# Kernel optimization log

Measured on AMD Instinct MI355X. Metric: run time of the kernel, lower is better.

The kernel has to match this reference:

```python
import jax, jax.numpy as jnp
import numpy as np

N = 20000
E = 320000
C = 16   # in_channels
G = 8    # growth_channels
H = 16   # kernel MLP hidden = RDB in_channels
DIM = 3
OMEGA = 100.0
BETA = 0.2


def _u(k, shape, s):
    return jax.random.uniform(k, shape, jnp.float32, -s, s)


def setup_inputs() -> dict:
    key = jax.random.key(0)
    ks = jax.random.split(key, 64)
    x = jax.random.normal(ks[0], (N, C), jnp.float32)
    pos = jax.random.normal(ks[1], (N, DIM), jnp.float32)
    # random edges with no self loops (add_remaining_self_loops appends them in reference)
    src = jax.random.randint(ks[2], (E,), 0, N)
    off = jax.random.randint(ks[3], (E,), 1, N)
    dst = (src + off) % N
    edge_index = jnp.stack([src, dst])
    d = {"x": x, "edge_index": edge_index, "pos": pos}
    ins = [C, C + G, C + 2 * G]
    outs = [G, G, C]
    i = 4
    for ci, (cin, cout) in enumerate(zip(ins, outs), 1):
        # SineLayer weights: uniform(-1/in_features, 1/in_features); biases ~ torch Linear default
        d[f"c{ci}_w0"] = _u(ks[i], (H, DIM + 1), 1.0 / (DIM + 1)); i += 1
        d[f"c{ci}_b0"] = _u(ks[i], (H,), 1.0 / np.sqrt(DIM + 1)); i += 1
        d[f"c{ci}_w1"] = _u(ks[i], (H, H), 1.0 / H); i += 1
        d[f"c{ci}_b1"] = _u(ks[i], (H,), 1.0 / np.sqrt(H)); i += 1
        d[f"c{ci}_w2"] = _u(ks[i], (H, H), 1.0 / H); i += 1
        d[f"c{ci}_b2"] = _u(ks[i], (H,), 1.0 / np.sqrt(H)); i += 1
        # final Linear(hidden -> in_size), stored transposed as [in_size, hidden]
        d[f"c{ci}_wl"] = _u(ks[i], (cin, H), 1.0 / np.sqrt(H)); i += 1
        d[f"c{ci}_bl"] = _u(ks[i], (cin,), 1.0 / np.sqrt(H)); i += 1
        d[f"c{ci}_bias"] = jnp.zeros((1, cout), jnp.float32); i += 1
    return d


def _edge_feat(pos, src, dst):
    # rel_pos = pos[dst] - pos[src]; spherical (rho, theta/pi, phi/pi), NaN at rho=0 -> 0
    rel = pos[dst] - pos[src]                              # [E,3]
    sq = jnp.sum(rel * rel, axis=1)
    zero = sq <= 0.0                                       # self loops
    rho = jnp.where(zero, 0.0, jnp.sqrt(jnp.where(zero, 1.0, sq)))
    theta = jnp.arctan2(jnp.where(zero, 0.0, rel[:, 1]), jnp.where(zero, 1.0, rel[:, 0]))
    phi = jnp.arcsin(jnp.clip(jnp.where(zero, 0.0, rel[:, 2]) / jnp.where(zero, 1.0, rho), -1.0, 1.0))
    return jnp.stack([rho, theta / jnp.pi, phi / jnp.pi], axis=1)  # [E,3]


def _gconv(feat, x, src, dst, n, out_ch, w0, b0, w1, b1, w2, b2, wl, bl, bias):
    # vectorized over output channels: channel index c is the 4th input of sin0
    base = feat @ w0[:, :3].T + b0                          # [E,H]
    ch = jnp.arange(out_ch, dtype=feat.dtype)               # [O]
    h = jnp.sin(OMEGA * (base[:, None, :] + ch[None, :, None] * w0[:, 3]))   # [E,O,H]
    h = jnp.sin(OMEGA * (jnp.einsum('eoh,gh->eog', h, w1) + b1))
    h = jnp.sin(OMEGA * (jnp.einsum('eoh,gh->eog', h, w2) + b2))
    xj = x[src]                                             # [E,in]
    # msg[e,o] = (Wl h[e,o] + bl) . x_j[e]  ==  h[e,o] . (Wl^T x_j[e]) + bl . x_j[e]
    msg = jnp.einsum('eoh,eh->eo', h, xj @ wl) + (xj @ bl)[:, None]
    return jax.ops.segment_sum(msg, dst, num_segments=n) + bias


def reference(x, edge_index, pos,
              c1_w0, c1_b0, c1_w1, c1_b1, c1_w2, c1_b2, c1_wl, c1_bl, c1_bias,
              c2_w0, c2_b0, c2_w1, c2_b1, c2_w2, c2_b2, c2_wl, c2_bl, c2_bias,
              c3_w0, c3_b0, c3_w1, c3_b1, c3_w2, c3_b2, c3_wl, c3_bl, c3_bias):
    n = x.shape[0]
    loop = jnp.arange(n, dtype=edge_index.dtype)
    src = jnp.concatenate([edge_index[0], loop])
    dst = jnp.concatenate([edge_index[1], loop])
    feat = _edge_feat(pos, src, dst)
    x1 = jax.nn.selu(_gconv(feat, x, src, dst, n, G, c1_w0, c1_b0, c1_w1, c1_b1, c1_w2, c1_b2, c1_wl, c1_bl, c1_bias))
    x2 = jax.nn.selu(_gconv(feat, jnp.concatenate([x, x1], 1), src, dst, n, G, c2_w0, c2_b0, c2_w1, c2_b1, c2_w2, c2_b2, c2_wl, c2_bl, c2_bias))
    x3 = jax.nn.selu(_gconv(feat, jnp.concatenate([x, x1, x2], 1), src, dst, n, C, c3_w0, c3_b0, c3_w1, c3_b1, c3_w2, c3_b2, c3_wl, c3_bl, c3_bias))
    return x + BETA * x3
```

## Files before the change

kernel.cpp:

```cpp
#include <hip/hip_runtime.h>
#include <math.h>

#define N_NODES 20000
#define N_EDGES 320000
#define HID 16
#define OMEGA 100.0f
#define BETA 0.2f
#define REVC 0.15915494309189535f

#define OFF_W0I 0
#define OFF_B1  64
#define OFF_B2  80
#define OFF_A2  128
#define OFF_WLH 384
#define OFF_WLL 640
#define OFF_AO  896
#define OFF_H2V 9088
#define P_SIZE  9472

typedef float  f32x4 __attribute__((ext_vector_type(4)));
typedef short  s16x8 __attribute__((ext_vector_type(8)));

__device__ __forceinline__ float sinrev(float x) { return __builtin_amdgcn_sinf(x); }
__device__ __forceinline__ float cosrev(float x) { return __builtin_amdgcn_cosf(x); }
__device__ __forceinline__ float fract_f(float x) { return __builtin_amdgcn_fractf(x); }

__device__ __forceinline__ float selu_f(float v) {
    const float a  = 1.6732632423543772f;
    const float sc = 1.0507009873554805f;
    return sc * (v > 0.f ? v : a * expm1f(v));
}

__device__ __forceinline__ f32x4 mfma16(s16x8 a, s16x8 b, f32x4 c) {
    return __builtin_amdgcn_mfma_f32_16x16x32_bf16(a, b, c, 0, 0, 0);
}

__device__ __forceinline__ unsigned pk_hi(float a, float b) {
    return (__float_as_uint(b) & 0xFFFF0000u) | (__float_as_uint(a) >> 16);
}
__device__ __forceinline__ float lo_of(float a) {
    return a - __uint_as_float(__float_as_uint(a) & 0xFFFF0000u);
}

union U4 { uint4 v; s16x8 s; };

struct PrepArgs {
    const float* w0[3]; const float* b0[3]; const float* w1[3]; const float* b1[3];
    const float* w2[3]; const float* b2[3]; const float* wl[3];
    float* P[3];
};

__global__ __launch_bounds__(256) void prep_kernel(PrepArgs A)
{
    const int INS[3]  = {16, 24, 32};
    const int OUTS[3] = {8, 8, 16};
    int c = blockIdx.x;
    int IN = INS[c], OUT = OUTS[c];
    const float* w0 = A.w0[c]; const float* b0 = A.b0[c];
    const float* w1 = A.w1[c]; const float* b1 = A.b1[c];
    const float* w2 = A.w2[c]; const float* b2 = A.b2[c];
    const float* wl = A.wl[c];
    float* P = A.P[c];
    unsigned* Pu = (unsigned*)P;

    __shared__ float W1s[256], W2s[256], cosB[256], sinB[256], w0c[16];
    int t = threadIdx.x;
    const float s = OMEGA * REVC;
    W1s[t] = s * w1[t];
    W2s[t] = s * w2[t];
    if (t < 16) w0c[t] = s * w0[t * 4 + 3];
    __syncthreads();

    if (t < 64) { int h = t >> 2, k = t & 3; P[t] = (k < 3) ? s * w0[h * 4 + k] : s * b0[h]; }
    if (t >= 64 && t < 80)  P[t] = s * b1[t - 64];
    if (t >= 80 && t < 96)  P[t] = s * b2[t - 80];

    if (t < OUT * 16) {
        int o = t >> 4, h = t & 15;
        float ang = fract_f((float)o * w0c[h]);
        cosB[t] = cosrev(ang);
        sinB[t] = sinrev(ang);
    }
    __syncthreads();

    if (t < 64) {
        int g = t & 15, q = t >> 4;
        float w[4], l[4];
#pragma unroll
        for (int j = 0; j < 4; j++) { w[j] = W2s[g * 16 + 4 * q + j]; l[j] = lo_of(w[j]); }
        ((uint4*)(Pu + OFF_A2))[t] = make_uint4(pk_hi(w[0], w[1]), pk_hi(w[2], w[3]),
                                                pk_hi(l[0], l[1]), pk_hi(l[2], l[3]));
    }
    if (t >= 64 && t < 128) {
        int lane = t - 64, g = lane & 15, q = lane >> 4;
        float v[8], l[8];
#pragma unroll
        for (int e = 0; e < 8; e++) {
            int i = 8 * q + e;
            v[e] = (i < IN) ? wl[i * 16 + g] : 0.f;
            l[e] = lo_of(v[e]);
        }
        ((uint4*)(Pu + OFF_WLH))[lane] = make_uint4(pk_hi(v[0], v[1]), pk_hi(v[2], v[3]),
                                                    pk_hi(v[4], v[5]), pk_hi(v[6], v[7]));
        ((uint4*)(Pu + OFF_WLL))[lane] = make_uint4(pk_hi(l[0], l[1]), pk_hi(l[2], l[3]),
                                                    pk_hi(l[4], l[5]), pk_hi(l[6], l[7]));
    }
    for (int idx = t; idx < OUT * 64; idx += 256) {
        int o = idx >> 6, lane = idx & 63, g = lane & 15, q = lane >> 4;
        float v[8], l[8];
#pragma unroll
        for (int e = 0; e < 8; e++) {
            int k = 8 * q + e;
            float a = (k < 16) ? W1s[g * 16 + k] * cosB[o * 16 + k]
                               : W1s[g * 16 + (k - 16)] * sinB[o * 16 + (k - 16)];
            v[e] = a; l[e] = lo_of(a);
        }
        ((uint4*)(Pu + OFF_AO + o * 512))[lane] =
            make_uint4(pk_hi(v[0], v[1]), pk_hi(v[2], v[3]), pk_hi(v[4], v[5]), pk_hi(v[6], v[7]));
        ((uint4*)(Pu + OFF_AO + o * 512 + 256))[lane] =
            make_uint4(pk_hi(l[0], l[1]), pk_hi(l[2], l[3]), pk_hi(l[4], l[5]), pk_hi(l[6], l[7]));
    }
    if (t < OUT) {
        float oc = (float)t;
        float h0[HID], h1[HID];
#pragma unroll
        for (int h = 0; h < HID; h++)
            h0[h] = sinrev(fract_f(fmaf(oc, w0c[h], s * b0[h])));
#pragma unroll
        for (int g = 0; g < HID; g++) {
            float sa = s * b1[g];
#pragma unroll
            for (int h = 0; h < HID; h++) sa += h0[h] * W1s[g * HID + h];
            h1[g] = sinrev(sa);
        }
#pragma unroll
        for (int g = 0; g < HID; g++) {
            float sa = s * b2[g];
#pragma unroll
            for (int h = 0; h < HID; h++) sa += h1[h] * W2s[g * HID + h];
            P[OFF_H2V + t * HID + g] = sinrev(sa);
        }
    }
}

__global__ __launch_bounds__(256) void fused_pre_kernel(
    const int* __restrict__ ei, const float* __restrict__ pos,
    const float* __restrict__ x,
    float4* __restrict__ feat, float* __restrict__ xcat,
    const float* __restrict__ wl1, const float* __restrict__ bl1,
    float* __restrict__ tb, float* __restrict__ blxb)
{
    int b = blockIdx.x;
    if (b < 1250) {
        int e = b * 256 + threadIdx.x;
        if (e >= N_EDGES) return;
        int s = ei[e], d = ei[N_EDGES + e];
        float rx = pos[d * 3 + 0] - pos[s * 3 + 0];
        float ry = pos[d * 3 + 1] - pos[s * 3 + 1];
        float rz = pos[d * 3 + 2] - pos[s * 3 + 2];
        float sq = rx * rx + ry * ry + rz * rz;
        float4 f = make_float4(0.f, 0.f, 0.f, 0.f);
        if (sq > 0.f) {
            float rho = sqrtf(sq);
            float th  = atan2f(ry, rx);
            float ph  = asinf(fminf(fmaxf(rz / rho, -1.f), 1.f));
            const float inv_pi = 0.31830988618379067f;
            f = make_float4(rho, th * inv_pi, ph * inv_pi, 0.f);
        }
        feat[e] = f;
    } else if (b < 2500) {
        int i = (b - 1250) * 256 + threadIdx.x;
        if (i >= N_NODES * 16) return;
        int n = i >> 4, cc = i & 15;
        xcat[n * 32 + cc] = x[i];
    } else {
        int n = (b - 2500) * 256 + threadIdx.x;
        if (n >= N_NODES) return;
        float tn[HID];
#pragma unroll
        for (int h = 0; h < HID; h++) tn[h] = 0.f;
        float bx = 0.f;
#pragma unroll
        for (int i = 0; i < 16; i++) {
            float xi = x[n * 16 + i];
            bx += bl1[i] * xi;
#pragma unroll
            for (int h = 0; h < HID; h++) tn[h] += wl1[i * 16 + h] * xi;
        }
#pragma unroll
        for (int h = 0; h < HID; h++) tb[n * 16 + h] = tn[h];
        blxb[n] = bx;
    }
}

template<int OUT, int IN>
__global__ __launch_bounds__(256) void conv_kernel(
    const int* __restrict__ ei, const float4* __restrict__ feat,
    const float* __restrict__ xcat, const float* __restrict__ P,
    const float* __restrict__ bl, float* __restrict__ acc)
{
    constexpr int L2O = (OUT == 16) ? 4 : 3;
    constexpr int EPI = 64 / OUT;
    constexpr int NI  = 16 / EPI;

    __shared__ float sm[4][16 * 17];
    const unsigned* Pu = (const unsigned*)P;
    int wslot = threadIdx.x >> 6;
    int wid  = (blockIdx.x * 256 + threadIdx.x) >> 6;
    int lane = threadIdx.x & 63;
    int e16 = lane & 15, q = lane >> 4;
    int e = wid * 16 + e16;
    int src = ei[e];
    int dst = ei[N_EDGES + e];
    float4 f = feat[e];

    float tr[8];
    {
        const float4* w0i = (const float4*)P;
        int hb = (q & 1) * 8;
#pragma unroll
        for (int j = 0; j < 8; j++) {
            float4 w = w0i[hb + j];
            float ang = fract_f(w.w + f.x * w.x + f.y * w.y + f.z * w.z);
            tr[j] = (q < 2) ? sinrev(ang) : cosrev(ang);
        }
    }
    U4 Bh, Bl;
    Bh.v = make_uint4(pk_hi(tr[0], tr[1]), pk_hi(tr[2], tr[3]),
                      pk_hi(tr[4], tr[5]), pk_hi(tr[6], tr[7]));
    Bl.v = make_uint4(pk_hi(lo_of(tr[0]), lo_of(tr[1])), pk_hi(lo_of(tr[2]), lo_of(tr[3])),
                      pk_hi(lo_of(tr[4]), lo_of(tr[5])), pk_hi(lo_of(tr[6]), lo_of(tr[7])));

    float xv[8];
#pragma unroll
    for (int j = 0; j < 8; j++) xv[j] = 0.f;
    if (8 * q < IN) {
        const f32x4* xr = (const f32x4*)(xcat + src * 32 + 8 * q);
        f32x4 x0 = xr[0], x1 = xr[1];
        xv[0] = x0[0]; xv[1] = x0[1]; xv[2] = x0[2]; xv[3] = x0[3];
        xv[4] = x1[0]; xv[5] = x1[1]; xv[6] = x1[2]; xv[7] = x1[3];
    }
    U4 Xh, Xl;
    Xh.v = make_uint4(pk_hi(xv[0], xv[1]), pk_hi(xv[2], xv[3]),
                      pk_hi(xv[4], xv[5]), pk_hi(xv[6], xv[7]));
    Xl.v = make_uint4(pk_hi(lo_of(xv[0]), lo_of(xv[1])), pk_hi(lo_of(xv[2]), lo_of(xv[3])),
                      pk_hi(lo_of(xv[4]), lo_of(xv[5])), pk_hi(lo_of(xv[6]), lo_of(xv[7])));
    U4 WLh, WLl;
    WLh.v = ((const uint4*)(Pu + OFF_WLH))[lane];
    WLl.v = ((const uint4*)(Pu + OFF_WLL))[lane];
    f32x4 T = {0.f, 0.f, 0.f, 0.f};
    T = mfma16(WLh.s, Xh.s, T);
    T = mfma16(WLh.s, Xl.s, T);
    T = mfma16(WLl.s, Xh.s, T);

    float bx = 0.f;
    if (8 * q < IN) {
        const f32x4* blr = (const f32x4*)(bl + 8 * q);
        f32x4 b0v = blr[0], b1v = blr[1];
        bx = b0v[0] * xv[0] + b0v[1] * xv[1] + b0v[2] * xv[2] + b0v[3] * xv[3]
           + b1v[0] * xv[4] + b1v[1] * xv[5] + b1v[2] * xv[6] + b1v[3] * xv[7];
    }
    bx += __shfl_xor(bx, 16);
    bx += __shfl_xor(bx, 32);

    U4 A2; A2.v = ((const uint4*)(Pu + OFF_A2))[lane];
    f32x4 c1 = *(const f32x4*)(P + OFF_B1 + 4 * q);
    f32x4 c2 = *(const f32x4*)(P + OFF_B2 + 4 * q);

#pragma unroll 2
    for (int o = 0; o < OUT; ++o) {
        U4 Ah, Al;
        Ah.v = ((const uint4*)(Pu + OFF_AO + o * 512))[lane];
        Al.v = ((const uint4*)(Pu + OFF_AO + o * 512 + 256))[lane];
        f32x4 D = c1;
        D = mfma16(Ah.s, Bh.s, D);
        D = mfma16(Ah.s, Bl.s, D);
        D = mfma16(Al.s, Bh.s, D);
        float h1[4];
#pragma unroll
        for (int j = 0; j < 4; j++) h1[j] = sinrev(D[j]);
        unsigned p0 = pk_hi(h1[0], h1[1]), p1 = pk_hi(h1[2], h1[3]);
        unsigned l0 = pk_hi(lo_of(h1[0]), lo_of(h1[1])), l1 = pk_hi(lo_of(h1[2]), lo_of(h1[3]));
        U4 Ph, Pl;
        Ph.v = make_uint4(p0, p1, p0, p1);
        Pl.v = make_uint4(l0, l1, l0, l1);
        f32x4 D2 = c2;
        D2 = mfma16(A2.s, Ph.s, D2);
        D2 = mfma16(A2.s, Pl.s, D2);
        float m = sinrev(D2[0]) * T[0] + sinrev(D2[1]) * T[1]
                + sinrev(D2[2]) * T[2] + sinrev(D2[3]) * T[3];
        m += __shfl_xor(m, 16);
        m += __shfl_xor(m, 32);
        if (lane < 16) sm[wslot][o * 17 + e16] = m + bx;
    }

    int oo = lane & (OUT - 1);
    int el = lane >> L2O;
#pragma unroll
    for (int j = 0; j < NI; j++) {
        int ej = j * EPI + el;
        int dj = __shfl(dst, ej);
        atomicAdd(&acc[dj * OUT + oo], sm[wslot][oo * 17 + ej]);
    }
}

template<int OUT, int CO>
__global__ __launch_bounds__(256) void finish_mid_kernel(
    const float* __restrict__ acc, const float* __restrict__ bias,
    const float* __restrict__ h2v,
    float* __restrict__ tb, float* __restrict__ blxb,
    float* __restrict__ xcat,
    const float* __restrict__ wlN, const float* __restrict__ blN)
{
    int n = blockIdx.x * 256 + threadIdx.x;
    if (n >= N_NODES) return;
    float trr[HID];
#pragma unroll
    for (int h = 0; h < HID; h++) trr[h] = tb[n * 16 + h];
    float bx = blxb[n];
    float xrow[CO + OUT];
#pragma unroll
    for (int i = 0; i < CO; i++) xrow[i] = xcat[n * 32 + i];
#pragma unroll
    for (int o = 0; o < OUT; o++) {
        float m = bx;
#pragma unroll
        for (int h = 0; h < HID; h++) m += h2v[o * 16 + h] * trr[h];
        float v = selu_f(acc[n * OUT + o] + bias[o] + m);
        xrow[CO + o] = v;
        xcat[n * 32 + CO + o] = v;
    }
    float tn[HID];
#pragma unroll
    for (int h = 0; h < HID; h++) tn[h] = 0.f;
    float bxn = 0.f;
#pragma unroll
    for (int i = 0; i < CO + OUT; i++) {
        float xi = xrow[i];
        bxn += blN[i] * xi;
#pragma unroll
        for (int h = 0; h < HID; h++) tn[h] += wlN[i * 16 + h] * xi;
    }
#pragma unroll
    for (int h = 0; h < HID; h++) tb[n * 16 + h] = tn[h];
    blxb[n] = bxn;
}

__global__ __launch_bounds__(256) void finish_out_kernel(
    const float* __restrict__ acc, const float* __restrict__ bias,
    const float* __restrict__ h2v,
    const float* __restrict__ tb, const float* __restrict__ blxb,
    const float* __restrict__ x, float* __restrict__ out)
{
    int n = blockIdx.x * 256 + threadIdx.x;
    if (n >= N_NODES) return;
    float trr[HID];
#pragma unroll
    for (int h = 0; h < HID; h++) trr[h] = tb[n * 16 + h];
    float bx = blxb[n];
#pragma unroll
    for (int c = 0; c < 16; c++) {
        float m = bx;
#pragma unroll
        for (int h = 0; h < HID; h++) m += h2v[c * 16 + h] * trr[h];
        out[n * 16 + c] = x[n * 16 + c] + BETA * selu_f(acc[n * 16 + c] + bias[c] + m);
    }
}

extern "C" void kernel_launch(void* const* d_in, const int* in_sizes, int n_in,
                              void* d_out, int out_size, void* d_ws, size_t ws_size,
                              hipStream_t stream)
{
    const float* x   = (const float*)d_in[0];
    const int*   ei  = (const int*)d_in[1];
    const float* pos = (const float*)d_in[2];

    const float* W[27];
    for (int i = 0; i < 27; i++) W[i] = (const float*)d_in[3 + i];

    float* ws    = (float*)d_ws;
    float4* feat = (float4*)ws;
    float* xcat  = ws + (size_t)N_EDGES * 4;
    float* acc1  = xcat + (size_t)N_NODES * 32;
    float* acc2  = acc1 + (size_t)N_NODES * 8;
    float* acc3  = acc2 + (size_t)N_NODES * 8;
    float* P1    = acc3 + (size_t)N_NODES * 16;
    float* P2    = P1 + P_SIZE;
    float* P3    = P2 + P_SIZE;
    float* tb    = P3 + P_SIZE;
    float* blxb  = tb + (size_t)N_NODES * 16;
    float* out   = (float*)d_out;

    hipMemsetAsync(acc1, 0, (size_t)N_NODES * 32 * sizeof(float), stream);

    PrepArgs pa;
    for (int c = 0; c < 3; c++) {
        pa.w0[c] = W[9 * c + 0]; pa.b0[c] = W[9 * c + 1];
        pa.w1[c] = W[9 * c + 2]; pa.b1[c] = W[9 * c + 3];
        pa.w2[c] = W[9 * c + 4]; pa.b2[c] = W[9 * c + 5];
        pa.wl[c] = W[9 * c + 6];
    }
    pa.P[0] = P1; pa.P[1] = P2; pa.P[2] = P3;

    dim3 blk(256);
    prep_kernel<<<3, blk, 0, stream>>>(pa);
    fused_pre_kernel<<<2579, blk, 0, stream>>>(ei, pos, x, feat, xcat, W[6], W[7], tb, blxb);

    conv_kernel<8, 16><<<5000, blk, 0, stream>>>(ei, feat, xcat, P1, W[7], acc1);
    finish_mid_kernel<8, 16><<<79, blk, 0, stream>>>(acc1, W[8], P1 + OFF_H2V, tb, blxb, xcat, W[15], W[16]);

    conv_kernel<8, 24><<<5000, blk, 0, stream>>>(ei, feat, xcat, P2, W[16], acc2);
    finish_mid_kernel<8, 24><<<79, blk, 0, stream>>>(acc2, W[17], P2 + OFF_H2V, tb, blxb, xcat, W[24], W[25]);

    conv_kernel<16, 32><<<5000, blk, 0, stream>>>(ei, feat, xcat, P3, W[25], acc3);
    finish_out_kernel<<<79, blk, 0, stream>>>(acc3, W[26], P3 + OFF_H2V, tb, blxb, x, out);
}
```

Measured before the change: 187.6 us.

## Process two edge groups per wave to reuse per-output weight fragments

Each wave now handles 32 edges as two 16-edge groups instead of one, so every per-output A-matrix fragment load feeds MFMAs for both groups. The next output's weight fragments are prefetched while the current one is computed, with the loop kept rolled. Grid size is halved to match. This cuts weight reloads and exposes more independent MFMA work per iteration, at the cost of more registers and fewer waves.

```diff
diff --git a/kernel.cpp b/kernel.cpp
--- a/kernel.cpp
+++ b/kernel.cpp
@@ -203,20 +203,34 @@
     constexpr int EPI = 64 / OUT;
     constexpr int NI  = 16 / EPI;
 
-    __shared__ float sm[4][16 * 17];
+    __shared__ float sm[4][2][16 * 17];
     const unsigned* Pu = (const unsigned*)P;
     int wslot = threadIdx.x >> 6;
     int wid  = (blockIdx.x * 256 + threadIdx.x) >> 6;
     int lane = threadIdx.x & 63;
     int e16 = lane & 15, q = lane >> 4;
-    int e = wid * 16 + e16;
-    int src = ei[e];
-    int dst = ei[N_EDGES + e];
-    float4 f = feat[e];
-
-    float tr[8];
-    {
-        const float4* w0i = (const float4*)P;
+
+    U4 WLh, WLl, A2;
+    WLh.v = ((const uint4*)(Pu + OFF_WLH))[lane];
+    WLl.v = ((const uint4*)(Pu + OFF_WLL))[lane];
+    A2.v  = ((const uint4*)(Pu + OFF_A2))[lane];
+    f32x4 c1 = *(const f32x4*)(P + OFF_B1 + 4 * q);
+    f32x4 c2 = *(const f32x4*)(P + OFF_B2 + 4 * q);
+    const float4* w0i = (const float4*)P;
+
+    U4 Bh[2], Bl[2];
+    f32x4 T[2];
+    float bx[2];
+    int dst[2];
+
+#pragma unroll
+    for (int gg = 0; gg < 2; gg++) {
+        int e = wid * 32 + gg * 16 + e16;
+        int src = ei[e];
+        dst[gg] = ei[N_EDGES + e];
+        float4 f = feat[e];
+
+        float tr[8];
         int hb = (q & 1) * 8;
 #pragma unroll
         for (int j = 0; j < 8; j++) {
@@ -224,83 +238,88 @@
             float ang = fract_f(w.w + f.x * w.x + f.y * w.y + f.z * w.z);
             tr[j] = (q < 2) ? sinrev(ang) : cosrev(ang);
         }
-    }
-    U4 Bh, Bl;
-    Bh.v = make_uint4(pk_hi(tr[0], tr[1]), pk_hi(tr[2], tr[3]),
-                      pk_hi(tr[4], tr[5]), pk_hi(tr[6], tr[7]));
-    Bl.v = make_uint4(pk_hi(lo_of(tr[0]), lo_of(tr[1])), pk_hi(lo_of(tr[2]), lo_of(tr[3])),
-                      pk_hi(lo_of(tr[4]), lo_of(tr[5])), pk_hi(lo_of(tr[6]), lo_of(tr[7])));
-
-    float xv[8];
-#pragma unroll
-    for (int j = 0; j < 8; j++) xv[j] = 0.f;
-    if (8 * q < IN) {
-        const f32x4* xr = (const f32x4*)(xcat + src * 32 + 8 * q);
-        f32x4 x0 = xr[0], x1 = xr[1];
-        xv[0] = x0[0]; xv[1] = x0[1]; xv[2] = x0[2]; xv[3] = x0[3];
-        xv[4] = x1[0]; xv[5] = x1[1]; xv[6] = x1[2]; xv[7] = x1[3];
-    }
-    U4 Xh, Xl;
-    Xh.v = make_uint4(pk_hi(xv[0], xv[1]), pk_hi(xv[2], xv[3]),
-                      pk_hi(xv[4], xv[5]), pk_hi(xv[6], xv[7]));
-    Xl.v = make_uint4(pk_hi(lo_of(xv[0]), lo_of(xv[1])), pk_hi(lo_of(xv[2]), lo_of(xv[3])),
-                      pk_hi(lo_of(xv[4]), lo_of(xv[5])), pk_hi(lo_of(xv[6]), lo_of(xv[7])));
-    U4 WLh, WLl;
-    WLh.v = ((const uint4*)(Pu + OFF_WLH))[lane];
-    WLl.v = ((const uint4*)(Pu + OFF_WLL))[lane];
-    f32x4 T = {0.f, 0.f, 0.f, 0.f};
-    T = mfma16(WLh.s, Xh.s, T);
-    T = mfma16(WLh.s, Xl.s, T);
-    T = mfma16(WLl.s, Xh.s, T);
-
-    float bx = 0.f;
-    if (8 * q < IN) {
-        const f32x4* blr = (const f32x4*)(bl + 8 * q);
-        f32x4 b0v = blr[0], b1v = blr[1];
-        bx = b0v[0] * xv[0] + b0v[1] * xv[1] + b0v[2] * xv[2] + b0v[3] * xv[3]
-           + b1v[0] * xv[4] + b1v[1] * xv[5] + b1v[2] * xv[6] + b1v[3] * xv[7];
-    }
-    bx += __shfl_xor(bx, 16);
-    bx += __shfl_xor(bx, 32);
-
-    U4 A2; A2.v = ((const uint4*)(Pu + OFF_A2))[lane];
-    f32x4 c1 = *(const f32x4*)(P + OFF_B1 + 4 * q);
-    f32x4 c2 = *(const f32x4*)(P + OFF_B2 + 4 * q);
-
-#pragma unroll 2
+        Bh[gg].v = make_uint4(pk_hi(tr[0], tr[1]), pk_hi(tr[2], tr[3]),
+                              pk_hi(tr[4], tr[5]), pk_hi(tr[6], tr[7]));
+        Bl[gg].v = make_uint4(pk_hi(lo_of(tr[0]), lo_of(tr[1])), pk_hi(lo_of(tr[2]), lo_of(tr[3])),
+                              pk_hi(lo_of(tr[4]), lo_of(tr[5])), pk_hi(lo_of(tr[6]), lo_of(tr[7])));
+
+        float xv[8];
+#pragma unroll
+        for (int j = 0; j < 8; j++) xv[j] = 0.f;
+        if (8 * q < IN) {
+            const f32x4* xr = (const f32x4*)(xcat + src * 32 + 8 * q);
+            f32x4 x0 = xr[0], x1 = xr[1];
+            xv[0] = x0[0]; xv[1] = x0[1]; xv[2] = x0[2]; xv[3] = x0[3];
+            xv[4] = x1[0]; xv[5] = x1[1]; xv[6] = x1[2]; xv[7] = x1[3];
+        }
+        U4 Xh, Xl;
+        Xh.v = make_uint4(pk_hi(xv[0], xv[1]), pk_hi(xv[2], xv[3]),
+                          pk_hi(xv[4], xv[5]), pk_hi(xv[6], xv[7]));
+        Xl.v = make_uint4(pk_hi(lo_of(xv[0]), lo_of(xv[1])), pk_hi(lo_of(xv[2]), lo_of(xv[3])),
+                          pk_hi(lo_of(xv[4]), lo_of(xv[5])), pk_hi(lo_of(xv[6]), lo_of(xv[7])));
+        f32x4 Tg = {0.f, 0.f, 0.f, 0.f};
+        Tg = mfma16(WLh.s, Xh.s, Tg);
+        Tg = mfma16(WLh.s, Xl.s, Tg);
+        Tg = mfma16(WLl.s, Xh.s, Tg);
+        T[gg] = Tg;
+
+        float b = 0.f;
+        if (8 * q < IN) {
+            const f32x4* blr = (const f32x4*)(bl + 8 * q);
+            f32x4 b0v = blr[0], b1v = blr[1];
+            b = b0v[0] * xv[0] + b0v[1] * xv[1] + b0v[2] * xv[2] + b0v[3] * xv[3]
+              + b1v[0] * xv[4] + b1v[1] * xv[5] + b1v[2] * xv[6] + b1v[3] * xv[7];
+        }
+        b += __shfl_xor(b, 16);
+        b += __shfl_xor(b, 32);
+        bx[gg] = b;
+    }
+
+    U4 Ah, Al, AhN, AlN;
+    Ah.v = ((const uint4*)(Pu + OFF_AO))[lane];
+    Al.v = ((const uint4*)(Pu + OFF_AO + 256))[lane];
+#pragma unroll 1
     for (int o = 0; o < OUT; ++o) {
-        U4 Ah, Al;
-        Ah.v = ((const uint4*)(Pu + OFF_AO + o * 512))[lane];
-        Al.v = ((const uint4*)(Pu + OFF_AO + o * 512 + 256))[lane];
-        f32x4 D = c1;
-        D = mfma16(Ah.s, Bh.s, D);
-        D = mfma16(Ah.s, Bl.s, D);
-        D = mfma16(Al.s, Bh.s, D);
-        float h1[4];
-#pragma unroll
-        for (int j = 0; j < 4; j++) h1[j] = sinrev(D[j]);
-        unsigned p0 = pk_hi(h1[0], h1[1]), p1 = pk_hi(h1[2], h1[3]);
-        unsigned l0 = pk_hi(lo_of(h1[0]), lo_of(h1[1])), l1 = pk_hi(lo_of(h1[2]), lo_of(h1[3]));
-        U4 Ph, Pl;
-        Ph.v = make_uint4(p0, p1, p0, p1);
-        Pl.v = make_uint4(l0, l1, l0, l1);
-        f32x4 D2 = c2;
-        D2 = mfma16(A2.s, Ph.s, D2);
-        D2 = mfma16(A2.s, Pl.s, D2);
-        float m = sinrev(D2[0]) * T[0] + sinrev(D2[1]) * T[1]
-                + sinrev(D2[2]) * T[2] + sinrev(D2[3]) * T[3];
-        m += __shfl_xor(m, 16);
-        m += __shfl_xor(m, 32);
-        if (lane < 16) sm[wslot][o * 17 + e16] = m + bx;
+        if (o + 1 < OUT) {
+            AhN.v = ((const uint4*)(Pu + OFF_AO + (o + 1) * 512))[lane];
+            AlN.v = ((const uint4*)(Pu + OFF_AO + (o + 1) * 512 + 256))[lane];
+        }
+#pragma unroll
+        for (int gg = 0; gg < 2; gg++) {
+            f32x4 D = c1;
+            D = mfma16(Ah.s, Bh[gg].s, D);
+            D = mfma16(Ah.s, Bl[gg].s, D);
+            D = mfma16(Al.s, Bh[gg].s, D);
+            float h1[4];
+#pragma unroll
+            for (int j = 0; j < 4; j++) h1[j] = sinrev(D[j]);
+            unsigned p0 = pk_hi(h1[0], h1[1]), p1 = pk_hi(h1[2], h1[3]);
+            unsigned l0 = pk_hi(lo_of(h1[0]), lo_of(h1[1])), l1 = pk_hi(lo_of(h1[2]), lo_of(h1[3]));
+            U4 Ph, Pl;
+            Ph.v = make_uint4(p0, p1, p0, p1);
+            Pl.v = make_uint4(l0, l1, l0, l1);
+            f32x4 D2 = c2;
+            D2 = mfma16(A2.s, Ph.s, D2);
+            D2 = mfma16(A2.s, Pl.s, D2);
+            float m = sinrev(D2[0]) * T[gg][0] + sinrev(D2[1]) * T[gg][1]
+                    + sinrev(D2[2]) * T[gg][2] + sinrev(D2[3]) * T[gg][3];
+            m += __shfl_xor(m, 16);
+            m += __shfl_xor(m, 32);
+            if (lane < 16) sm[wslot][gg][o * 17 + e16] = m + bx[gg];
+        }
+        Ah = AhN; Al = AlN;
     }
 
     int oo = lane & (OUT - 1);
     int el = lane >> L2O;
 #pragma unroll
-    for (int j = 0; j < NI; j++) {
-        int ej = j * EPI + el;
-        int dj = __shfl(dst, ej);
-        atomicAdd(&acc[dj * OUT + oo], sm[wslot][oo * 17 + ej]);
+    for (int gg = 0; gg < 2; gg++) {
+#pragma unroll
+        for (int j = 0; j < NI; j++) {
+            int ej = j * EPI + el;
+            int dj = __shfl(dst[gg], ej);
+            atomicAdd(&acc[dj * OUT + oo], sm[wslot][gg][oo * 17 + ej]);
+        }
     }
 }
 
@@ -406,12 +425,12 @@
     prep_kernel<<<3, blk, 0, stream>>>(pa);
     fused_pre_kernel<<<2579, blk, 0, stream>>>(ei, pos, x, feat, xcat, W[6], W[7], tb, blxb);
 
-    conv_kernel<8, 16><<<5000, blk, 0, stream>>>(ei, feat, xcat, P1, W[7], acc1);
+    conv_kernel<8, 16><<<2500, blk, 0, stream>>>(ei, feat, xcat, P1, W[7], acc1);
     finish_mid_kernel<8, 16><<<79, blk, 0, stream>>>(acc1, W[8], P1 + OFF_H2V, tb, blxb, xcat, W[15], W[16]);
 
-    conv_kernel<8, 24><<<5000, blk, 0, stream>>>(ei, feat, xcat, P2, W[16], acc2);
+    conv_kernel<8, 24><<<2500, blk, 0, stream>>>(ei, feat, xcat, P2, W[16], acc2);
     finish_mid_kernel<8, 24><<<79, blk, 0, stream>>>(acc2, W[17], P2 + OFF_H2V, tb, blxb, xcat, W[24], W[25]);
 
-    conv_kernel<16, 32><<<5000, blk, 0, stream>>>(ei, feat, xcat, P3, W[25], acc3);
+    conv_kernel<16, 32><<<2500, blk, 0, stream>>>(ei, feat, xcat, P3, W[25], acc3);
     finish_out_kernel<<<79, blk, 0, stream>>>(acc3, W[26], P3 + OFF_H2V, tb, blxb, x, out);
 }
```

New measurement: 197.4 us. 5.3% more time.

## Split conv output channels across two wave slices and prefetch per-output weights

Applied to the files above, without the earlier changes.

The conv kernel gains an output-channel count per wave (OCNT). For layers 1 and 3 the grid doubles so that two waves handle disjoint halves of the output channels for the same 16-edge group. This raises the number of waves in flight but recomputes the first-layer sine features and the Wl·x products in both slices. The per-output A-matrix fragments are also software-prefetched one iteration ahead, and the shared-memory tile shrinks to 8 outputs.

```diff
diff --git a/kernel.cpp b/kernel.cpp
--- a/kernel.cpp
+++ b/kernel.cpp
@@ -193,23 +193,26 @@
     }
 }
 
-template<int OUT, int IN>
+template<int OUT, int IN, int OCNT>
 __global__ __launch_bounds__(256) void conv_kernel(
     const int* __restrict__ ei, const float4* __restrict__ feat,
     const float* __restrict__ xcat, const float* __restrict__ P,
     const float* __restrict__ bl, float* __restrict__ acc)
 {
-    constexpr int L2O = (OUT == 16) ? 4 : 3;
-    constexpr int EPI = 64 / OUT;
+    constexpr int L2OC = (OCNT == 4) ? 2 : ((OCNT == 8) ? 3 : 4);
+    constexpr int EPI = 64 / OCNT;
     constexpr int NI  = 16 / EPI;
 
-    __shared__ float sm[4][16 * 17];
+    __shared__ float sm[4][8 * 17];
     const unsigned* Pu = (const unsigned*)P;
     int wslot = threadIdx.x >> 6;
-    int wid  = (blockIdx.x * 256 + threadIdx.x) >> 6;
+    int gid  = blockIdx.x * 4 + wslot;
+    int slice = (gid >= 20000) ? 1 : 0;
+    int group = gid - slice * 20000;
+    int obase = slice * OCNT;
     int lane = threadIdx.x & 63;
     int e16 = lane & 15, q = lane >> 4;
-    int e = wid * 16 + e16;
+    int e = group * 16 + e16;
     int src = ei[e];
     int dst = ei[N_EDGES + e];
     float4 f = feat[e];
@@ -267,11 +270,15 @@
     f32x4 c1 = *(const f32x4*)(P + OFF_B1 + 4 * q);
     f32x4 c2 = *(const f32x4*)(P + OFF_B2 + 4 * q);
 
+    U4 Ah, Al, AhN, AlN;
+    Ah.v = ((const uint4*)(Pu + OFF_AO + obase * 512))[lane];
+    Al.v = ((const uint4*)(Pu + OFF_AO + obase * 512 + 256))[lane];
 #pragma unroll 2
-    for (int o = 0; o < OUT; ++o) {
-        U4 Ah, Al;
-        Ah.v = ((const uint4*)(Pu + OFF_AO + o * 512))[lane];
-        Al.v = ((const uint4*)(Pu + OFF_AO + o * 512 + 256))[lane];
+    for (int lo = 0; lo < OCNT; ++lo) {
+        if (lo + 1 < OCNT) {
+            AhN.v = ((const uint4*)(Pu + OFF_AO + (obase + lo + 1) * 512))[lane];
+            AlN.v = ((const uint4*)(Pu + OFF_AO + (obase + lo + 1) * 512 + 256))[lane];
+        }
         f32x4 D = c1;
         D = mfma16(Ah.s, Bh.s, D);
         D = mfma16(Ah.s, Bl.s, D);
@@ -291,16 +298,17 @@
                 + sinrev(D2[2]) * T[2] + sinrev(D2[3]) * T[3];
         m += __shfl_xor(m, 16);
         m += __shfl_xor(m, 32);
-        if (lane < 16) sm[wslot][o * 17 + e16] = m + bx;
-    }
-
-    int oo = lane & (OUT - 1);
-    int el = lane >> L2O;
+        if (lane < 16) sm[wslot][lo * 17 + e16] = m + bx;
+        Ah = AhN; Al = AlN;
+    }
+
+    int oo = lane & (OCNT - 1);
+    int el = lane >> L2OC;
 #pragma unroll
     for (int j = 0; j < NI; j++) {
         int ej = j * EPI + el;
         int dj = __shfl(dst, ej);
-        atomicAdd(&acc[dj * OUT + oo], sm[wslot][oo * 17 + ej]);
+        atomicAdd(&acc[dj * OUT + obase + oo], sm[wslot][oo * 17 + ej]);
     }
 }
 
@@ -406,12 +414,12 @@
     prep_kernel<<<3, blk, 0, stream>>>(pa);
     fused_pre_kernel<<<2579, blk, 0, stream>>>(ei, pos, x, feat, xcat, W[6], W[7], tb, blxb);
 
-    conv_kernel<8, 16><<<5000, blk, 0, stream>>>(ei, feat, xcat, P1, W[7], acc1);
+    conv_kernel<8, 16, 4><<<10000, blk, 0, stream>>>(ei, feat, xcat, P1, W[7], acc1);
     finish_mid_kernel<8, 16><<<79, blk, 0, stream>>>(acc1, W[8], P1 + OFF_H2V, tb, blxb, xcat, W[15], W[16]);
 
-    conv_kernel<8, 24><<<5000, blk, 0, stream>>>(ei, feat, xcat, P2, W[16], acc2);
+    conv_kernel<8, 24, 8><<<5000, blk, 0, stream>>>(ei, feat, xcat, P2, W[16], acc2);
     finish_mid_kernel<8, 24><<<79, blk, 0, stream>>>(acc2, W[17], P2 + OFF_H2V, tb, blxb, xcat, W[24], W[25]);
 
-    conv_kernel<16, 32><<<5000, blk, 0, stream>>>(ei, feat, xcat, P3, W[25], acc3);
+    conv_kernel<16, 32, 8><<<10000, blk, 0, stream>>>(ei, feat, xcat, P3, W[25], acc3);
     finish_out_kernel<<<79, blk, 0, stream>>>(acc3, W[26], P3 + OFF_H2V, tb, blxb, x, out);
 }
```

Result: slower. 201.8 us (+7.6%).
